# Optimization experiments

Measured on AMD Instinct MI355X. Metric: run time of the kernel, lower is better.

Reference implementation:

```python
import jax, jax.numpy as jnp
import numpy as np

B, N_IN, D_IN, N_OUT, D_OUT = 16, 256, 128, 128, 64
W_INIT_CONST = float(np.sqrt(N_OUT / (D_IN * N_IN)))


def setup_inputs() -> dict:
    key = jax.random.key(0)
    k1, k2, k3 = jax.random.split(key, 3)
    x = jax.random.normal(k1, (B, N_IN, D_IN), dtype=jnp.float32)
    current_act = jax.random.uniform(k2, (B, N_IN), dtype=jnp.float32)
    W = W_INIT_CONST * jax.random.normal(k3, (N_IN, D_IN, N_OUT, D_OUT), dtype=jnp.float32)
    return {"input": x, "current_act": current_act, "W": W, "num_iter": 1}


def reference(input, current_act, W, num_iter):
    scale = 1.0 / np.sqrt(D_OUT)
    # votes[b,n,m,d] = sum_a input[b,n,a] * W[n,a,m,d]  -- the big bilinear product,
    # computed once and reused for score computation and the final weighted reduce.
    votes = jnp.einsum('bna,namd->bnmd', input, W)  # [B, N_IN, N_OUT, D_OUT]

    # next_capsule_value is None -> uniform query_key = softmax(zeros) = 1/N_OUT
    ncv = votes.sum(axis=1) / N_OUT  # [B, N_OUT, D_OUT]

    # next_act is None -> mean activation broadcast to all output capsules
    next_act = jnp.broadcast_to(current_act.mean(axis=1, keepdims=True), (B, N_OUT))

    # attention-like routing coefficients
    scores = jnp.einsum('bnmd,bmd->bnm', votes, ncv) * scale  # [B, N_IN, N_OUT]
    qk = jax.nn.softmax(scores, axis=2) * next_act[:, None, :]
    qk = qk / (qk.sum(axis=2, keepdims=True) + 1e-10)

    # weighted reduce of votes, gated by input activations
    next_capsule_value = jnp.einsum('bnm,bn,bnmd->bmd', qk, current_act, votes)
    return (next_capsule_value, next_act, qk)
```

## Files before the change

### kernel.cpp

```cpp
#include <hip/hip_runtime.h>
#include <hip/hip_bf16.h>
#include <cstdint>


#define BB 16
#define N_IN 256
#define D_IN 128
#define N_OUT 128
#define D_OUT 64
#define MD (N_OUT * D_OUT)
#define NPB 2
#define NCH 32

typedef float f4v __attribute__((ext_vector_type(4)));

__global__ __launch_bounds__(256) void pass0_xT(
    const float* __restrict__ x, float* __restrict__ xT)
{
    const int idx = blockIdx.x * 256 + threadIdx.x;
    const int b = idx & 15;
    const int a = (idx >> 4) & 127;
    const int n = idx >> 11;
    xT[idx] = x[((size_t)b * N_IN + n) * D_IN + a];
}

__global__ __launch_bounds__(256, 3) void pass1_votes(
    const float* __restrict__ xT, const float* __restrict__ W,
    uint2* __restrict__ votes4)
{
    __shared__ float xs[NPB * D_IN * BB];
    const int t = threadIdx.x;
    const int chunk = blockIdx.x;
    const int ng = blockIdx.y;
    const int j = chunk * 1024 + t * 4;

    {
        const float4* src = reinterpret_cast<const float4*>(xT + ((size_t)ng * NPB << 11));
        float4* dst = reinterpret_cast<float4*>(xs);
#pragma unroll
        for (int r = 0; r < 4; ++r) dst[r * 256 + t] = src[r * 256 + t];
    }
    __syncthreads();

    for (int ni = 0; ni < NPB; ++ni) {
        const int n = ng * NPB + ni;
        const f4v* __restrict__ Wp =
            reinterpret_cast<const f4v*>(W + (size_t)n * D_IN * MD + j);

        float acc[BB][4];
#pragma unroll
        for (int b = 0; b < BB; ++b) {
            acc[b][0] = 0.f; acc[b][1] = 0.f; acc[b][2] = 0.f; acc[b][3] = 0.f;
        }

        f4v wq[8];
#pragma unroll
        for (int p = 0; p < 8; ++p)
            wq[p] = __builtin_nontemporal_load(Wp + (size_t)p * (MD / 4));

        for (int ab = 0; ab < D_IN; ab += 8) {
            const bool more = (ab + 8) < D_IN;
#pragma unroll
            for (int p = 0; p < 8; ++p) {
                const int a = ab + p;
                const f4v w = wq[p];
                if (more)
                    wq[p] = __builtin_nontemporal_load(Wp + (size_t)(a + 8) * (MD / 4));
                const float4* xa = reinterpret_cast<const float4*>(xs + (ni * D_IN + a) * BB);
                const float4 x0 = xa[0], x1 = xa[1], x2 = xa[2], x3 = xa[3];
                const float xv[BB] = {x0.x, x0.y, x0.z, x0.w, x1.x, x1.y, x1.z, x1.w,
                                      x2.x, x2.y, x2.z, x2.w, x3.x, x3.y, x3.z, x3.w};
#pragma unroll
                for (int b = 0; b < BB; ++b) {
                    acc[b][0] = fmaf(xv[b], w[0], acc[b][0]);
                    acc[b][1] = fmaf(xv[b], w[1], acc[b][1]);
                    acc[b][2] = fmaf(xv[b], w[2], acc[b][2]);
                    acc[b][3] = fmaf(xv[b], w[3], acc[b][3]);
                }
            }
        }

#pragma unroll
        for (int b = 0; b < BB; ++b) {
            union { __hip_bfloat16 h[4]; uint2 u; } pk;
            pk.h[0] = __float2bfloat16(acc[b][0]);
            pk.h[1] = __float2bfloat16(acc[b][1]);
            pk.h[2] = __float2bfloat16(acc[b][2]);
            pk.h[3] = __float2bfloat16(acc[b][3]);
            votes4[(((size_t)b * N_IN + n) * MD + j) >> 2] = pk.u;
        }
    }
}

__global__ __launch_bounds__(256) void pass_ncv_part(
    const uint32_t* __restrict__ votes2, float* __restrict__ ncv_part)
{
    const int t = threadIdx.x;
    const int jc = blockIdx.x;
    const int nh = blockIdx.y;
    const int b  = blockIdx.z;
    const int j = jc * 1024 + t * 4;

    const uint2* vp = reinterpret_cast<const uint2*>(votes2) +
                      ((((size_t)b * N_IN + (size_t)nh * 64) * MD + j) >> 2);
    float s0 = 0.f, s1 = 0.f, s2 = 0.f, s3 = 0.f;
#pragma unroll 8
    for (int n = 0; n < 64; ++n) {
        const uint2 u = vp[(size_t)n * (MD / 4)];
        s0 += __uint_as_float(u.x << 16);
        s1 += __uint_as_float(u.x & 0xffff0000u);
        s2 += __uint_as_float(u.y << 16);
        s3 += __uint_as_float(u.y & 0xffff0000u);
    }
    float4 o; o.x = s0; o.y = s1; o.z = s2; o.w = s3;
    *reinterpret_cast<float4*>(ncv_part + ((size_t)nh * BB + b) * MD + j) = o;
}

__global__ __launch_bounds__(256) void pass3_route(
    const __hip_bfloat16* __restrict__ votes, const float* __restrict__ ncv_part,
    const float* __restrict__ act, float* __restrict__ out_part,
    float* __restrict__ next_act_out, float* __restrict__ qk_out)
{
    __shared__ float red[4];
    __shared__ float aw[4];
    const int t = threadIdx.x;
    const int b = blockIdx.x;
    const int nc = blockIdx.y;
    const int m = t >> 1;
    const int half = t & 1;

    float av = act[b * N_IN + t];
#pragma unroll
    for (int off = 32; off; off >>= 1) av += __shfl_xor(av, off);
    if ((t & 63) == 0) aw[t >> 6] = av;
    __syncthreads();
    const float amean = (aw[0] + aw[1] + aw[2] + aw[3]) * (1.f / 256.f);
    const float qs = amean / (amean + 1e-10f);
    if (nc == 0 && half == 0) next_act_out[b * N_OUT + m] = amean;

    float nv[32], oacc[32];
    {
        const float4* p0 = reinterpret_cast<const float4*>(ncv_part + ((size_t)0 * BB + b) * MD + t * 32);
        const float4* p1 = reinterpret_cast<const float4*>(ncv_part + ((size_t)1 * BB + b) * MD + t * 32);
        const float4* p2 = reinterpret_cast<const float4*>(ncv_part + ((size_t)2 * BB + b) * MD + t * 32);
        const float4* p3 = reinterpret_cast<const float4*>(ncv_part + ((size_t)3 * BB + b) * MD + t * 32);
#pragma unroll
        for (int q = 0; q < 8; ++q) {
            const float4 a0 = p0[q], a1 = p1[q], a2 = p2[q], a3 = p3[q];
            nv[4 * q + 0] = (a0.x + a1.x) + (a2.x + a3.x);
            nv[4 * q + 1] = (a0.y + a1.y) + (a2.y + a3.y);
            nv[4 * q + 2] = (a0.z + a1.z) + (a2.z + a3.z);
            nv[4 * q + 3] = (a0.w + a1.w) + (a2.w + a3.w);
        }
#pragma unroll
        for (int i = 0; i < 32; ++i) { nv[i] *= (1.f / (float)N_OUT); oacc[i] = 0.f; }
    }

    const uint4* vbase = reinterpret_cast<const uint4*>(
        votes + (size_t)b * ((size_t)N_IN * MD) + (size_t)(nc * 8) * MD + t * 32);
    const size_t nstride = MD / 8;

    uint4 buf[4];
#pragma unroll
    for (int q = 0; q < 4; ++q) buf[q] = vbase[q];

    for (int ni = 0; ni < 8; ++ni) {
        const int n = nc * 8 + ni;
        float vv[32];
#pragma unroll
        for (int q = 0; q < 4; ++q) {
            const uint32_t ww[4] = {buf[q].x, buf[q].y, buf[q].z, buf[q].w};
#pragma unroll
            for (int k = 0; k < 4; ++k) {
                vv[8 * q + 2 * k]     = __uint_as_float(ww[k] << 16);
                vv[8 * q + 2 * k + 1] = __uint_as_float(ww[k] & 0xffff0000u);
            }
        }
        if (ni < 7) {
            const uint4* vn = vbase + (size_t)(ni + 1) * nstride;
#pragma unroll
            for (int q = 0; q < 4; ++q) buf[q] = vn[q];
        }

        float p0 = 0.f, p1 = 0.f, p2 = 0.f, p3 = 0.f;
#pragma unroll
        for (int i = 0; i < 8; ++i) {
            p0 = fmaf(vv[4 * i + 0], nv[4 * i + 0], p0);
            p1 = fmaf(vv[4 * i + 1], nv[4 * i + 1], p1);
            p2 = fmaf(vv[4 * i + 2], nv[4 * i + 2], p2);
            p3 = fmaf(vv[4 * i + 3], nv[4 * i + 3], p3);
        }
        float sp = (p0 + p1) + (p2 + p3);
        sp += __shfl_xor(sp, 1);
        sp *= 0.125f;

        const float p = __expf(sp);
        float s = p;
#pragma unroll
        for (int off = 32; off; off >>= 1) s += __shfl_xor(s, off);
        if ((t & 63) == 0) red[t >> 6] = s;
        __syncthreads();
        const float ssum = (red[0] + red[1] + red[2] + red[3]) * 0.5f;
        __syncthreads();

        const float qk = (p / ssum) * qs;
        if (half == 0) qk_out[((size_t)(b * N_IN + n) << 7) + m] = qk;

        const float c = qk * act[b * N_IN + n];
#pragma unroll
        for (int i = 0; i < 32; ++i) oacc[i] = fmaf(c, vv[i], oacc[i]);
    }

    float4* op = reinterpret_cast<float4*>(out_part + ((size_t)nc * BB + b) * MD + t * 32);
#pragma unroll
    for (int q = 0; q < 8; ++q) {
        float4 o; o.x = oacc[4 * q]; o.y = oacc[4 * q + 1];
        o.z = oacc[4 * q + 2]; o.w = oacc[4 * q + 3];
        op[q] = o;
    }
}

__global__ __launch_bounds__(256) void combine_out0(
    const float* __restrict__ out_part, float* __restrict__ out0)
{
    const int idx = blockIdx.x * 256 + threadIdx.x;
    const int b = idx >> 11;
    const int v4 = idx & 2047;
    const float4* p = reinterpret_cast<const float4*>(out_part);
    float4 s = {0.f, 0.f, 0.f, 0.f};
#pragma unroll 8
    for (int nc = 0; nc < NCH; ++nc) {
        const float4 f = p[((size_t)nc * BB + b) * (MD / 4) + v4];
        s.x += f.x; s.y += f.y; s.z += f.z; s.w += f.w;
    }
    reinterpret_cast<float4*>(out0)[idx] = s;
}

extern "C" void kernel_launch(void* const* d_in, const int* in_sizes, int n_in,
                              void* d_out, int out_size, void* d_ws, size_t ws_size,
                              hipStream_t stream)
{
    const float* x   = (const float*)d_in[0];
    const float* act = (const float*)d_in[1];
    const float* W   = (const float*)d_in[2];

    float* out      = (float*)d_out;
    float* out0     = out;
    float* next_act = out + 131072;
    float* qk_out   = out + 131072 + 2048;

    __hip_bfloat16* votes = (__hip_bfloat16*)d_ws;
    float* ncv_part = (float*)((char*)d_ws + (size_t)67108864);
    float* out_part = (float*)((char*)d_ws + (size_t)67108864 + 2097152);
    float* xT       = (float*)((char*)d_ws + (size_t)67108864 + 2097152 + 16777216);

    pass0_xT<<<2048, 256, 0, stream>>>(x, xT);
    pass1_votes<<<dim3(8, 128), 256, 0, stream>>>(xT, W, (uint2*)votes);
    pass_ncv_part<<<dim3(8, 4, 16), 256, 0, stream>>>((const uint32_t*)votes, ncv_part);
    pass3_route<<<dim3(16, NCH), 256, 0, stream>>>(votes, ncv_part, act, out_part,
                                                   next_act, qk_out);
    combine_out0<<<128, 256, 0, stream>>>(out_part, out0);
}
```

Baseline: 270.9 us.

## Use packed FMA in votes kernel and split routing/ncv across more blocks

The votes GEMM inner loop is rewritten to use 2-wide float vector FMAs, pairing two batch rows per operation so the compiler can emit packed FMA instructions. The ncv partial-sum and routing kernels are split into twice as many chunks along the input-capsule axis to raise grid parallelism. The combine kernel is relaunched with 128-thread blocks. In exchange, the partial buffers double in size, each routing block reloads ncv from eight partials, and the combine step sums more partials.

```diff
diff --git a/kernel.cpp b/kernel.cpp
--- a/kernel.cpp
+++ b/kernel.cpp
@@ -10,9 +10,11 @@
 #define D_OUT 64
 #define MD (N_OUT * D_OUT)
 #define NPB 2
-#define NCH 32
+#define NCH 64
+#define NHS 8
 
 typedef float f4v __attribute__((ext_vector_type(4)));
+typedef float f2v __attribute__((ext_vector_type(2)));
 
 __global__ __launch_bounds__(256) void pass0_xT(
     const float* __restrict__ x, float* __restrict__ xT)
@@ -47,11 +49,11 @@
         const f4v* __restrict__ Wp =
             reinterpret_cast<const f4v*>(W + (size_t)n * D_IN * MD + j);
 
-        float acc[BB][4];
-#pragma unroll
-        for (int b = 0; b < BB; ++b) {
-            acc[b][0] = 0.f; acc[b][1] = 0.f; acc[b][2] = 0.f; acc[b][3] = 0.f;
-        }
+        f2v acc[8][4];
+#pragma unroll
+        for (int bp = 0; bp < 8; ++bp)
+#pragma unroll
+            for (int k = 0; k < 4; ++k) acc[bp][k] = f2v{0.f, 0.f};
 
         f4v wq[8];
 #pragma unroll
@@ -68,14 +70,17 @@
                     wq[p] = __builtin_nontemporal_load(Wp + (size_t)(a + 8) * (MD / 4));
                 const float4* xa = reinterpret_cast<const float4*>(xs + (ni * D_IN + a) * BB);
                 const float4 x0 = xa[0], x1 = xa[1], x2 = xa[2], x3 = xa[3];
-                const float xv[BB] = {x0.x, x0.y, x0.z, x0.w, x1.x, x1.y, x1.z, x1.w,
-                                      x2.x, x2.y, x2.z, x2.w, x3.x, x3.y, x3.z, x3.w};
-#pragma unroll
-                for (int b = 0; b < BB; ++b) {
-                    acc[b][0] = fmaf(xv[b], w[0], acc[b][0]);
-                    acc[b][1] = fmaf(xv[b], w[1], acc[b][1]);
-                    acc[b][2] = fmaf(xv[b], w[2], acc[b][2]);
-                    acc[b][3] = fmaf(xv[b], w[3], acc[b][3]);
+                const f2v xp[8] = {f2v{x0.x, x0.y}, f2v{x0.z, x0.w},
+                                   f2v{x1.x, x1.y}, f2v{x1.z, x1.w},
+                                   f2v{x2.x, x2.y}, f2v{x2.z, x2.w},
+                                   f2v{x3.x, x3.y}, f2v{x3.z, x3.w}};
+                const f2v wd[4] = {f2v{w[0], w[0]}, f2v{w[1], w[1]},
+                                   f2v{w[2], w[2]}, f2v{w[3], w[3]}};
+#pragma unroll
+                for (int bp = 0; bp < 8; ++bp) {
+#pragma unroll
+                    for (int k = 0; k < 4; ++k)
+                        acc[bp][k] = __builtin_elementwise_fma(xp[bp], wd[k], acc[bp][k]);
                 }
             }
         }
@@ -83,10 +88,10 @@
 #pragma unroll
         for (int b = 0; b < BB; ++b) {
             union { __hip_bfloat16 h[4]; uint2 u; } pk;
-            pk.h[0] = __float2bfloat16(acc[b][0]);
-            pk.h[1] = __float2bfloat16(acc[b][1]);
-            pk.h[2] = __float2bfloat16(acc[b][2]);
-            pk.h[3] = __float2bfloat16(acc[b][3]);
+            pk.h[0] = __float2bfloat16(acc[b >> 1][0][b & 1]);
+            pk.h[1] = __float2bfloat16(acc[b >> 1][1][b & 1]);
+            pk.h[2] = __float2bfloat16(acc[b >> 1][2][b & 1]);
+            pk.h[3] = __float2bfloat16(acc[b >> 1][3][b & 1]);
             votes4[(((size_t)b * N_IN + n) * MD + j) >> 2] = pk.u;
         }
     }
@@ -102,10 +107,10 @@
     const int j = jc * 1024 + t * 4;
 
     const uint2* vp = reinterpret_cast<const uint2*>(votes2) +
-                      ((((size_t)b * N_IN + (size_t)nh * 64) * MD + j) >> 2);
+                      ((((size_t)b * N_IN + (size_t)nh * 32) * MD + j) >> 2);
     float s0 = 0.f, s1 = 0.f, s2 = 0.f, s3 = 0.f;
 #pragma unroll 8
-    for (int n = 0; n < 64; ++n) {
+    for (int n = 0; n < 32; ++n) {
         const uint2 u = vp[(size_t)n * (MD / 4)];
         s0 += __uint_as_float(u.x << 16);
         s1 += __uint_as_float(u.x & 0xffff0000u);
@@ -140,32 +145,33 @@
 
     float nv[32], oacc[32];
     {
-        const float4* p0 = reinterpret_cast<const float4*>(ncv_part + ((size_t)0 * BB + b) * MD + t * 32);
-        const float4* p1 = reinterpret_cast<const float4*>(ncv_part + ((size_t)1 * BB + b) * MD + t * 32);
-        const float4* p2 = reinterpret_cast<const float4*>(ncv_part + ((size_t)2 * BB + b) * MD + t * 32);
-        const float4* p3 = reinterpret_cast<const float4*>(ncv_part + ((size_t)3 * BB + b) * MD + t * 32);
-#pragma unroll
-        for (int q = 0; q < 8; ++q) {
-            const float4 a0 = p0[q], a1 = p1[q], a2 = p2[q], a3 = p3[q];
-            nv[4 * q + 0] = (a0.x + a1.x) + (a2.x + a3.x);
-            nv[4 * q + 1] = (a0.y + a1.y) + (a2.y + a3.y);
-            nv[4 * q + 2] = (a0.z + a1.z) + (a2.z + a3.z);
-            nv[4 * q + 3] = (a0.w + a1.w) + (a2.w + a3.w);
+#pragma unroll
+        for (int i = 0; i < 32; ++i) nv[i] = 0.f;
+#pragma unroll
+        for (int h = 0; h < NHS; ++h) {
+            const float4* ph = reinterpret_cast<const float4*>(
+                ncv_part + ((size_t)h * BB + b) * MD + t * 32);
+#pragma unroll
+            for (int q = 0; q < 8; ++q) {
+                const float4 f = ph[q];
+                nv[4 * q + 0] += f.x; nv[4 * q + 1] += f.y;
+                nv[4 * q + 2] += f.z; nv[4 * q + 3] += f.w;
+            }
         }
 #pragma unroll
         for (int i = 0; i < 32; ++i) { nv[i] *= (1.f / (float)N_OUT); oacc[i] = 0.f; }
     }
 
     const uint4* vbase = reinterpret_cast<const uint4*>(
-        votes + (size_t)b * ((size_t)N_IN * MD) + (size_t)(nc * 8) * MD + t * 32);
+        votes + (size_t)b * ((size_t)N_IN * MD) + (size_t)(nc * 4) * MD + t * 32);
     const size_t nstride = MD / 8;
 
     uint4 buf[4];
 #pragma unroll
     for (int q = 0; q < 4; ++q) buf[q] = vbase[q];
 
-    for (int ni = 0; ni < 8; ++ni) {
-        const int n = nc * 8 + ni;
+    for (int ni = 0; ni < 4; ++ni) {
+        const int n = nc * 4 + ni;
         float vv[32];
 #pragma unroll
         for (int q = 0; q < 4; ++q) {
@@ -176,7 +182,7 @@
                 vv[8 * q + 2 * k + 1] = __uint_as_float(ww[k] & 0xffff0000u);
             }
         }
-        if (ni < 7) {
+        if (ni < 3) {
             const uint4* vn = vbase + (size_t)(ni + 1) * nstride;
 #pragma unroll
             for (int q = 0; q < 4; ++q) buf[q] = vn[q];
@@ -220,10 +226,10 @@
     }
 }
 
-__global__ __launch_bounds__(256) void combine_out0(
+__global__ __launch_bounds__(128) void combine_out0(
     const float* __restrict__ out_part, float* __restrict__ out0)
 {
-    const int idx = blockIdx.x * 256 + threadIdx.x;
+    const int idx = blockIdx.x * 128 + threadIdx.x;
     const int b = idx >> 11;
     const int v4 = idx & 2047;
     const float4* p = reinterpret_cast<const float4*>(out_part);
@@ -251,13 +257,13 @@
 
     __hip_bfloat16* votes = (__hip_bfloat16*)d_ws;
     float* ncv_part = (float*)((char*)d_ws + (size_t)67108864);
-    float* out_part = (float*)((char*)d_ws + (size_t)67108864 + 2097152);
-    float* xT       = (float*)((char*)d_ws + (size_t)67108864 + 2097152 + 16777216);
+    float* out_part = (float*)((char*)d_ws + (size_t)67108864 + 4194304);
+    float* xT       = (float*)((char*)d_ws + (size_t)67108864 + 4194304 + 33554432);
 
     pass0_xT<<<2048, 256, 0, stream>>>(x, xT);
     pass1_votes<<<dim3(8, 128), 256, 0, stream>>>(xT, W, (uint2*)votes);
-    pass_ncv_part<<<dim3(8, 4, 16), 256, 0, stream>>>((const uint32_t*)votes, ncv_part);
+    pass_ncv_part<<<dim3(8, NHS, 16), 256, 0, stream>>>((const uint32_t*)votes, ncv_part);
     pass3_route<<<dim3(16, NCH), 256, 0, stream>>>(votes, ncv_part, act, out_part,
                                                    next_act, qk_out);
-    combine_out0<<<128, 256, 0, stream>>>(out_part, out0);
-}
+    combine_out0<<<256, 128, 0, stream>>>(out_part, out0);
+}
```

Measured after the change: 281.5 us. 3.9% more time.
